# Optimization experiments

Measured on AMD Instinct MI355X. Metric: run time of the kernel, lower is better.

Reference implementation:

```python
import jax, jax.numpy as jnp
import numpy as np

# ---- static module config (HashEncoder defaults) ----
INPUT_DIM = 3
NUM_LEVELS = 16
LEVEL_DIM = 2
PER_LEVEL_SCALE = 2.0
BASE_RES = 16
LOG2_HASHMAP = 19
MAX_PARAMS = 2 ** LOG2_HASHMAP
S = np.log2(PER_LEVEL_SCALE)  # log2 of per-level scale, as in the CUDA kernel
B_POINTS = 1048576

# per-level table offsets, exactly as in HashEncoder.__init__
_offs = [0]
_off = 0
for _i in range(NUM_LEVELS):
    _res = int(np.ceil(BASE_RES * PER_LEVEL_SCALE ** _i))
    _p = min(MAX_PARAMS, (_res + 1) ** INPUT_DIM)
    _p = int(_p / 8) * 8
    _off += _p
    _offs.append(_off)
OFFSETS = np.array(_offs, dtype=np.int64)
N_ENTRIES = _off  # 7132272

# spatial hash primes from torch-ngp fast_hash (first 3 dims)
PRIMES = np.array([1, 2654435761, 805459861], dtype=np.uint32)


def _encode_level(inputs, emb_level, level, hashmap_size):
    """One resolution level: hash 8 corners, gather, trilinear-interp. inputs: [B,3] in [0,1]."""
    scale = np.float32(np.exp2(level * S) * BASE_RES - 1.0)
    resolution = int(np.ceil(scale)) + 1
    pos = inputs * scale + 0.5
    pos_grid = jnp.floor(pos)
    frac = pos - pos_grid                    # [B,3] trilinear fractions
    pg = pos_grid.astype(jnp.uint32)         # [B,3] base corner
    # kernel hashes whenever the dense grid would exceed the (rounded) table size
    use_hash = (resolution + 1) ** INPUT_DIM > hashmap_size
    hs = np.uint32(hashmap_size)
    out = jnp.zeros((inputs.shape[0], LEVEL_DIM), dtype=inputs.dtype)
    for c in range(2 ** INPUT_DIM):          # 8 corners
        bits = np.array([(c >> d) & 1 for d in range(INPUT_DIM)], dtype=np.uint32)
        w = jnp.prod(jnp.where(bits.astype(bool), frac, 1.0 - frac), axis=-1)  # [B]
        corner = pg + bits                   # [B,3] uint32
        if use_hash:
            h = corner * PRIMES              # uint32 wrap-around multiply
            idx = h[:, 0] ^ h[:, 1] ^ h[:, 2]
        else:
            stride = np.uint32(resolution + 1)
            idx = corner[:, 0] + corner[:, 1] * stride + corner[:, 2] * (stride * stride)
        idx = (idx % hs).astype(jnp.int32)
        out = out + w[:, None] * emb_level[idx]  # irregular gather [B,C]
    return out


def setup_inputs() -> dict:
    key = jax.random.key(0)
    k1, k2 = jax.random.split(key)
    xyz = jax.random.uniform(k1, (B_POINTS, INPUT_DIM), dtype=jnp.float32)
    # reset_parameters: uniform(-1e-4, 1e-4)
    embeddings = jax.random.uniform(k2, (N_ENTRIES, LEVEL_DIM), dtype=jnp.float32,
                                    minval=-1e-4, maxval=1e-4)
    return {"xyz": xyz, "embeddings": embeddings, "normalize": 0}


def reference(xyz, embeddings, normalize):
    # normalize == 0 -> use raw coords (kernel expects [0,1]^3), matching normalize=False path
    inputs = xyz.reshape(-1, INPUT_DIM)
    outs = []
    for l in range(NUM_LEVELS):
        o0, o1 = int(OFFSETS[l]), int(OFFSETS[l + 1])
        outs.append(_encode_level(inputs, embeddings[o0:o1], l, o1 - o0))
    # equivalent to outputs.permute(1,0,2).reshape(B, L*C)
    return jnp.concatenate(outs, axis=-1)
```

## Files before the change

kernel.cpp:

```cpp
#include <hip/hip_runtime.h>
#include <hip/hip_fp16.h>

#define NLEVELS 16
#define BLOCK 256
#define PPT1 4
#define PPT 2

struct HashParams {
    unsigned offs[NLEVELS + 1];
    unsigned hsize[NLEVELS];
    unsigned hash_bits;
    unsigned pow2_bits;
};

__global__ void __launch_bounds__(BLOCK)
hashenc_conv(const float4* __restrict__ emb2, uint2* __restrict__ tab16, int n2)
{
    const int i = blockIdx.x * BLOCK + threadIdx.x;
    if (i < n2) {
        const float4 v = emb2[i];
        const __half2 a = __floats2half2_rn(v.x, v.y);
        const __half2 b = __floats2half2_rn(v.z, v.w);
        tab16[i] = make_uint2(*(const unsigned*)&a, *(const unsigned*)&b);
    }
}

__global__ void __launch_bounds__(BLOCK)
hashenc_pass1_h(const float* __restrict__ xyz,
                const unsigned* __restrict__ tab16,
                unsigned* __restrict__ ws,
                HashParams p, int np, int bpl_shift)
{
    const int l = blockIdx.x >> bpl_shift;
    const int chunk = blockIdx.x & ((1 << bpl_shift) - 1);
    const int tid = threadIdx.x;

    __shared__ float sxyz[BLOCK * PPT1 * 3];
    {
        const float4* __restrict__ src =
            (const float4*)(xyz + (size_t)chunk * (BLOCK * PPT1) * 3);
        float4* __restrict__ dst = (float4*)sxyz;
#pragma unroll
        for (int i = tid; i < (BLOCK * PPT1 * 3) / 4; i += BLOCK)
            dst[i] = src[i];
    }
    __syncthreads();

    const unsigned hs = p.hsize[l];
    const unsigned* __restrict__ tab = tab16 + p.offs[l];
    const float scale = (float)((16u << l) - 1u);
    const bool is_pow2 = (p.pow2_bits >> l) & 1u;
    unsigned* __restrict__ wl = ws + (size_t)l * np;

    unsigned raw[PPT1][8];
    unsigned selba[PPT1];
    float fxa[PPT1], fya[PPT1], fza[PPT1];

#pragma unroll
    for (int s = 0; s < PPT1; ++s) {
        const int lp = s * BLOCK + tid;
        const float x = sxyz[lp * 3 + 0];
        const float y = sxyz[lp * 3 + 1];
        const float z = sxyz[lp * 3 + 2];
        const float px = x * scale + 0.5f;
        const float py = y * scale + 0.5f;
        const float pz = z * scale + 0.5f;
        const float gx = floorf(px), gy = floorf(py), gz = floorf(pz);
        fxa[s] = px - gx; fya[s] = py - gy; fza[s] = pz - gz;
        const unsigned ix = (unsigned)gx, iy = (unsigned)gy, iz = (unsigned)gz;

        const unsigned hy0 = iy * 2654435761u;
        const unsigned hz0 = iz * 805459861u;
        const unsigned hy1 = hy0 + 2654435761u;
        const unsigned hz1 = hz0 + 805459861u;
        const unsigned hyz[4] = { hy0 ^ hz0, hy1 ^ hz0, hy0 ^ hz1, hy1 ^ hz1 };

        unsigned selb = 0u;
        if (is_pow2) {
            const unsigned m = hs - 1u;
            if (!(ix & 1u)) {
#pragma unroll
                for (int q = 0; q < 4; ++q) {
                    const unsigned v0 = (ix ^ hyz[q]) & m;
                    const uint2 pr = *reinterpret_cast<const uint2*>(tab + (v0 & ~1u));
                    raw[s][2 * q]     = pr.x;
                    raw[s][2 * q + 1] = pr.y;
                    selb |= (v0 & 1u) << q;
                }
            } else {
#pragma unroll
                for (int q = 0; q < 4; ++q) {
                    raw[s][2 * q]     = tab[(ix ^ hyz[q]) & m];
                    raw[s][2 * q + 1] = tab[((ix + 1u) ^ hyz[q]) & m];
                }
            }
        } else {
#pragma unroll
            for (int q = 0; q < 4; ++q) {
                raw[s][2 * q]     = tab[(ix ^ hyz[q]) % hs];
                raw[s][2 * q + 1] = tab[((ix + 1u) ^ hyz[q]) % hs];
            }
        }
        selba[s] = selb;
    }

#pragma unroll
    for (int s = 0; s < PPT1; ++s) {
        const float fx = fxa[s], fy = fya[s], fz = fza[s];
        const float wxv[2] = {1.0f - fx, fx};
        const float wyv[2] = {1.0f - fy, fy};
        const float wzv[2] = {1.0f - fz, fz};
        const unsigned selb = selba[s];
        float o0 = 0.0f, o1 = 0.0f;
#pragma unroll
        for (int q = 0; q < 4; ++q) {
            const unsigned r0 = raw[s][2 * q], r1 = raw[s][2 * q + 1];
            const bool sw = (selb >> q) & 1u;
            const unsigned ua = sw ? r1 : r0;
            const unsigned ub = sw ? r0 : r1;
            const float2 ea = __half22float2(*reinterpret_cast<const __half2*>(&ua));
            const float2 eb = __half22float2(*reinterpret_cast<const __half2*>(&ub));
            const float wq = wyv[q & 1] * wzv[q >> 1];
            const float w0 = wxv[0] * wq, w1 = wxv[1] * wq;
            o0 = fmaf(w0, ea.x, o0); o1 = fmaf(w0, ea.y, o1);
            o0 = fmaf(w1, eb.x, o0); o1 = fmaf(w1, eb.y, o1);
        }
        const int pidx = chunk * (BLOCK * PPT1) + s * BLOCK + tid;
        const __half2 ph = __floats2half2_rn(o0, o1);
        wl[pidx] = *(const unsigned*)&ph;
    }
}

__global__ void __launch_bounds__(BLOCK)
hashenc_pass2_h(const unsigned* __restrict__ ws, float* __restrict__ out, int np)
{
    __shared__ float lds[BLOCK * 33];
    const int tid = threadIdx.x;
    const int p0 = blockIdx.x * BLOCK;

#pragma unroll
    for (int l = 0; l < NLEVELS; ++l) {
        const unsigned u = ws[(size_t)l * np + p0 + tid];
        const float2 v = __half22float2(*reinterpret_cast<const __half2*>(&u));
        lds[tid * 33 + 2 * l + 0] = v.x;
        lds[tid * 33 + 2 * l + 1] = v.y;
    }
    __syncthreads();
    float* __restrict__ ochunk = out + (size_t)blockIdx.x * (BLOCK * 32);
#pragma unroll
    for (int k = 0; k < 32; ++k) {
        const int flat = k * BLOCK + tid;
        const float v = lds[(flat >> 5) * 33 + (flat & 31)];
        __builtin_nontemporal_store(v, ochunk + flat);
    }
}

__global__ void __launch_bounds__(BLOCK)
hashenc_pass1_f32(const float* __restrict__ xyz,
                  const float* __restrict__ emb,
                  float2* __restrict__ ws,
                  HashParams p, int np, int bpl_shift)
{
    const int l = blockIdx.x >> bpl_shift;
    const int chunk = blockIdx.x & ((1 << bpl_shift) - 1);
    const int tid = threadIdx.x;

    __shared__ float sxyz[BLOCK * PPT * 3];
    {
        const float4* __restrict__ src =
            (const float4*)(xyz + (size_t)chunk * (BLOCK * PPT) * 3);
        float4* __restrict__ dst = (float4*)sxyz;
#pragma unroll
        for (int i = tid; i < (BLOCK * PPT * 3) / 4; i += BLOCK)
            dst[i] = src[i];
    }
    __syncthreads();

    const unsigned hs = p.hsize[l];
    const float2* __restrict__ tab = (const float2*)emb + p.offs[l];
    const float scale = (float)((16u << l) - 1u);
    const bool do_hash = (p.hash_bits >> l) & 1u;
    const bool is_pow2 = (p.pow2_bits >> l) & 1u;
    float2* __restrict__ wl = ws + (size_t)l * np;

#pragma unroll
    for (int s = 0; s < PPT; ++s) {
        const int lp = s * BLOCK + tid;
        const int pidx = chunk * (BLOCK * PPT) + lp;
        const float x = sxyz[lp * 3 + 0];
        const float y = sxyz[lp * 3 + 1];
        const float z = sxyz[lp * 3 + 2];
        const float px = x * scale + 0.5f;
        const float py = y * scale + 0.5f;
        const float pz = z * scale + 0.5f;
        const float gx = floorf(px), gy = floorf(py), gz = floorf(pz);
        const float fx = px - gx, fy = py - gy, fz = pz - gz;
        const unsigned ix = (unsigned)gx, iy = (unsigned)gy, iz = (unsigned)gz;
        const float wxv[2] = {1.0f - fx, fx};
        const float wyv[2] = {1.0f - fy, fy};
        const float wzv[2] = {1.0f - fz, fz};
        float o0 = 0.0f, o1 = 0.0f;
        unsigned idx[8];
        if (do_hash) {
            const unsigned hy0 = iy * 2654435761u;
            const unsigned hz0 = iz * 805459861u;
            const unsigned hy1 = hy0 + 2654435761u;
            const unsigned hz1 = hz0 + 805459861u;
            if (is_pow2) {
                const unsigned m = hs - 1u;
#pragma unroll
                for (int c = 0; c < 8; ++c)
                    idx[c] = ((ix + (c & 1)) ^ ((c & 2) ? hy1 : hy0) ^ ((c & 4) ? hz1 : hz0)) & m;
            } else {
#pragma unroll
                for (int c = 0; c < 8; ++c)
                    idx[c] = ((ix + (c & 1)) ^ ((c & 2) ? hy1 : hy0) ^ ((c & 4) ? hz1 : hz0)) % hs;
            }
        } else {
            const unsigned stride = (16u << l) + 1u;
#pragma unroll
            for (int c = 0; c < 8; ++c) {
                const unsigned lin = (ix + (c & 1))
                                   + (iy + ((c >> 1) & 1)) * stride
                                   + (iz + ((c >> 2) & 1)) * stride * stride;
                idx[c] = lin % hs;
            }
        }
        float2 e[8];
#pragma unroll
        for (int c = 0; c < 8; ++c) e[c] = tab[idx[c]];
#pragma unroll
        for (int c = 0; c < 8; ++c) {
            const float w = wxv[c & 1] * wyv[(c >> 1) & 1] * wzv[(c >> 2) & 1];
            o0 = fmaf(w, e[c].x, o0);
            o1 = fmaf(w, e[c].y, o1);
        }
        wl[pidx] = make_float2(o0, o1);
    }
}

__global__ void __launch_bounds__(BLOCK)
hashenc_pass2(const float2* __restrict__ ws, float* __restrict__ out, int np)
{
    __shared__ float lds[BLOCK * 33];
    const int tid = threadIdx.x;
    const int p0 = blockIdx.x * BLOCK;

#pragma unroll
    for (int l = 0; l < NLEVELS; ++l) {
        const float2 v = ws[(size_t)l * np + p0 + tid];
        lds[tid * 33 + 2 * l + 0] = v.x;
        lds[tid * 33 + 2 * l + 1] = v.y;
    }
    __syncthreads();
    float* __restrict__ ochunk = out + (size_t)blockIdx.x * (BLOCK * 32);
#pragma unroll
    for (int k = 0; k < 32; ++k) {
        const int flat = k * BLOCK + tid;
        const float v = lds[(flat >> 5) * 33 + (flat & 31)];
        __builtin_nontemporal_store(v, ochunk + flat);
    }
}

__global__ void __launch_bounds__(BLOCK)
hashenc_fwd(const float* __restrict__ xyz,
            const float* __restrict__ emb,
            float* __restrict__ out,
            HashParams p)
{
    const int tid = threadIdx.x;
    const long b = (long)blockIdx.x * BLOCK + tid;
    __shared__ float lds[BLOCK * 33];

    const float x = xyz[b * 3 + 0];
    const float y = xyz[b * 3 + 1];
    const float z = xyz[b * 3 + 2];

#pragma unroll
    for (int l = 0; l < NLEVELS; ++l) {
        const float scale = (float)((16u << l) - 1u);
        const float px = x * scale + 0.5f;
        const float py = y * scale + 0.5f;
        const float pz = z * scale + 0.5f;
        const float gx = floorf(px), gy = floorf(py), gz = floorf(pz);
        const float fx = px - gx, fy = py - gy, fz = pz - gz;
        const unsigned ix = (unsigned)gx, iy = (unsigned)gy, iz = (unsigned)gz;
        const unsigned hs = p.hsize[l];
        const float2* __restrict__ tab = (const float2*)emb + p.offs[l];

        unsigned idx[8];
        if ((p.hash_bits >> l) & 1u) {
            const unsigned hy0 = iy * 2654435761u;
            const unsigned hz0 = iz * 805459861u;
            const unsigned hy1 = hy0 + 2654435761u;
            const unsigned hz1 = hz0 + 805459861u;
            if ((p.pow2_bits >> l) & 1u) {
                const unsigned m = hs - 1u;
#pragma unroll
                for (int c = 0; c < 8; ++c)
                    idx[c] = ((ix + (c & 1)) ^ ((c & 2) ? hy1 : hy0) ^ ((c & 4) ? hz1 : hz0)) & m;
            } else {
#pragma unroll
                for (int c = 0; c < 8; ++c)
                    idx[c] = ((ix + (c & 1)) ^ ((c & 2) ? hy1 : hy0) ^ ((c & 4) ? hz1 : hz0)) % hs;
            }
        } else {
            const unsigned stride = (16u << l) + 1u;
#pragma unroll
            for (int c = 0; c < 8; ++c) {
                const unsigned lin = (ix + (c & 1))
                                   + (iy + ((c >> 1) & 1)) * stride
                                   + (iz + ((c >> 2) & 1)) * stride * stride;
                idx[c] = lin % hs;
            }
        }

        float2 e[8];
#pragma unroll
        for (int c = 0; c < 8; ++c) e[c] = tab[idx[c]];

        const float wx[2] = {1.0f - fx, fx};
        const float wy[2] = {1.0f - fy, fy};
        const float wz[2] = {1.0f - fz, fz};
        float o0 = 0.0f, o1 = 0.0f;
#pragma unroll
        for (int c = 0; c < 8; ++c) {
            const float w = wx[c & 1] * wy[(c >> 1) & 1] * wz[(c >> 2) & 1];
            o0 = fmaf(w, e[c].x, o0);
            o1 = fmaf(w, e[c].y, o1);
        }
        lds[tid * 33 + l * 2 + 0] = o0;
        lds[tid * 33 + l * 2 + 1] = o1;
    }

    __syncthreads();
    float* __restrict__ ochunk = out + (long)blockIdx.x * (BLOCK * 32);
#pragma unroll
    for (int k = 0; k < 32; ++k) {
        const int flat = k * BLOCK + tid;
        const float v = lds[(flat >> 5) * 33 + (flat & 31)];
        __builtin_nontemporal_store(v, ochunk + flat);
    }
}

extern "C" void kernel_launch(void* const* d_in, const int* in_sizes, int n_in,
                              void* d_out, int out_size, void* d_ws, size_t ws_size,
                              hipStream_t stream) {
    const float* xyz = (const float*)d_in[0];
    const float* emb = (const float*)d_in[1];
    float* out = (float*)d_out;
    const int B = in_sizes[0] / 3;

    HashParams p;
    p.offs[0] = 0;
    unsigned hash_bits = 0, pow2_bits = 0;
    long off = 0;
    for (int i = 0; i < NLEVELS; ++i) {
        const long res = 16L << i;
        const long dense = (res + 1) * (res + 1) * (res + 1);
        long t = dense < (1L << 19) ? dense : (1L << 19);
        t = (t / 8) * 8;
        p.hsize[i] = (unsigned)t;
        off += t;
        p.offs[i + 1] = (unsigned)off;
        if (dense > t) hash_bits |= (1u << i);
        if ((t & (t - 1)) == 0) pow2_bits |= (1u << i);
    }
    p.hash_bits = hash_bits;
    p.pow2_bits = pow2_bits;

    const long nent = off;
    const size_t need_ws16 = (size_t)B * NLEVELS * 4;
    const size_t need_h = need_ws16 + (size_t)nent * 4;
    const size_t need_f32 = (size_t)B * NLEVELS * sizeof(float2);
    const bool shape1_ok = (B % (BLOCK * PPT1)) == 0 && (B % BLOCK) == 0;
    const bool shape2_ok = (B % (BLOCK * PPT)) == 0 && (B % BLOCK) == 0;
    const bool all_hashed = (hash_bits == ((1u << NLEVELS) - 1u));

    if (shape1_ok && all_hashed && ws_size >= need_h) {
        unsigned* tab16 = (unsigned*)((char*)d_ws + need_ws16);
        const int n2 = (int)(nent / 2);
        hashenc_conv<<<dim3((n2 + BLOCK - 1) / BLOCK), dim3(BLOCK), 0, stream>>>(
            (const float4*)emb, (uint2*)tab16, n2);
        int bpl_shift = 0;
        while ((1 << bpl_shift) * (BLOCK * PPT1) < B) ++bpl_shift;
        const int bpl = 1 << bpl_shift;
        hashenc_pass1_h<<<dim3(NLEVELS * bpl), dim3(BLOCK), 0, stream>>>(
            xyz, tab16, (unsigned*)d_ws, p, B, bpl_shift);
        hashenc_pass2_h<<<dim3(B / BLOCK), dim3(BLOCK), 0, stream>>>(
            (const unsigned*)d_ws, out, B);
    } else if (shape2_ok && ws_size >= need_f32) {
        int bpl_shift = 0;
        while ((1 << bpl_shift) * (BLOCK * PPT) < B) ++bpl_shift;
        const int bpl = 1 << bpl_shift;
        hashenc_pass1_f32<<<dim3(NLEVELS * bpl), dim3(BLOCK), 0, stream>>>(
            xyz, emb, (float2*)d_ws, p, B, bpl_shift);
        hashenc_pass2<<<dim3(B / BLOCK), dim3(BLOCK), 0, stream>>>(
            (const float2*)d_ws, out, B);
    } else {
        hashenc_fwd<<<dim3(B / BLOCK), dim3(BLOCK), 0, stream>>>(xyz, emb, out, p);
    }
}
```

Before: 485.9 us.

## Encode two coarsest levels with LDS-staged hash table chunks in separate kernel

Adds a kernel that handles levels 0 and 1 by staging each level's fp16 table in 12288-entry chunks in shared memory. Every point scans all chunks and accumulates only the corners whose index falls inside the current chunk. The main per-level kernel now starts at level 2 and launches fewer blocks. The aim is to replace scattered global gathers on the small coarse tables with LDS reads, at the cost of recomputing hashes and reloading xyz from global memory once per chunk, plus one extra kernel launch.

Result: slower. 503.2 us (+3.6%).

```diff
diff --git a/kernel.cpp b/kernel.cpp
--- a/kernel.cpp
+++ b/kernel.cpp
@@ -5,6 +5,9 @@
 #define BLOCK 256
 #define PPT1 4
 #define PPT 2
+#define CCHUNK 12288
+#define PPT_C 8
+#define NCOARSE 2
 
 struct HashParams {
     unsigned offs[NLEVELS + 1];
@@ -26,12 +29,90 @@
 }
 
 __global__ void __launch_bounds__(BLOCK)
+hashenc_coarse(const float* __restrict__ xyz,
+               const unsigned* __restrict__ tab16,
+               unsigned* __restrict__ ws,
+               HashParams p, int np, int cblk_shift)
+{
+    __shared__ unsigned stab[CCHUNK];
+    const int l = blockIdx.x >> cblk_shift;
+    const int blk = blockIdx.x & ((1 << cblk_shift) - 1);
+    const int tid = threadIdx.x;
+
+    const unsigned hs = p.hsize[l];
+    const unsigned* __restrict__ tab = tab16 + p.offs[l];
+    const float scale = (float)((16u << l) - 1u);
+    unsigned* __restrict__ wl = ws + (size_t)l * np;
+    const int nchunks = (int)((hs + CCHUNK - 1) / CCHUNK);
+    const int base = blk * (BLOCK * PPT_C);
+
+    float acc0[PPT_C], acc1[PPT_C];
+#pragma unroll
+    for (int s = 0; s < PPT_C; ++s) { acc0[s] = 0.0f; acc1[s] = 0.0f; }
+
+    for (int c = 0; c < nchunks; ++c) {
+        const unsigned c0 = (unsigned)c * CCHUNK;
+        const unsigned cend = (c0 + CCHUNK < hs) ? c0 + CCHUNK : hs;
+        __syncthreads();
+        for (int i = tid; i < (int)(cend - c0); i += BLOCK)
+            stab[i] = tab[c0 + i];
+        __syncthreads();
+
+#pragma unroll
+        for (int s = 0; s < PPT_C; ++s) {
+            const int pidx = base + s * BLOCK + tid;
+            const float x = xyz[pidx * 3 + 0];
+            const float y = xyz[pidx * 3 + 1];
+            const float z = xyz[pidx * 3 + 2];
+            const float px = x * scale + 0.5f;
+            const float py = y * scale + 0.5f;
+            const float pz = z * scale + 0.5f;
+            const float gx = floorf(px), gy = floorf(py), gz = floorf(pz);
+            const float fx = px - gx, fy = py - gy, fz = pz - gz;
+            const unsigned ix = (unsigned)gx, iy = (unsigned)gy, iz = (unsigned)gz;
+            const unsigned hy0 = iy * 2654435761u;
+            const unsigned hz0 = iz * 805459861u;
+            const unsigned hy1 = hy0 + 2654435761u;
+            const unsigned hz1 = hz0 + 805459861u;
+            const unsigned hyz[4] = { hy0 ^ hz0, hy1 ^ hz0, hy0 ^ hz1, hy1 ^ hz1 };
+            const float wxv[2] = {1.0f - fx, fx};
+            const float wyv[2] = {1.0f - fy, fy};
+            const float wzv[2] = {1.0f - fz, fz};
+            float o0 = acc0[s], o1 = acc1[s];
+#pragma unroll
+            for (int q = 0; q < 4; ++q) {
+                const float wq = wyv[q & 1] * wzv[q >> 1];
+#pragma unroll
+                for (int cx = 0; cx < 2; ++cx) {
+                    const unsigned idx = ((ix + (unsigned)cx) ^ hyz[q]) % hs;
+                    if (idx >= c0 && idx < cend) {
+                        const unsigned u = stab[idx - c0];
+                        const float2 e = __half22float2(*reinterpret_cast<const __half2*>(&u));
+                        const float w = wxv[cx] * wq;
+                        o0 = fmaf(w, e.x, o0);
+                        o1 = fmaf(w, e.y, o1);
+                    }
+                }
+            }
+            acc0[s] = o0; acc1[s] = o1;
+        }
+    }
+
+#pragma unroll
+    for (int s = 0; s < PPT_C; ++s) {
+        const int pidx = base + s * BLOCK + tid;
+        const __half2 ph = __floats2half2_rn(acc0[s], acc1[s]);
+        wl[pidx] = *(const unsigned*)&ph;
+    }
+}
+
+__global__ void __launch_bounds__(BLOCK)
 hashenc_pass1_h(const float* __restrict__ xyz,
                 const unsigned* __restrict__ tab16,
                 unsigned* __restrict__ ws,
                 HashParams p, int np, int bpl_shift)
 {
-    const int l = blockIdx.x >> bpl_shift;
+    const int l = NCOARSE + (blockIdx.x >> bpl_shift);
     const int chunk = blockIdx.x & ((1 << bpl_shift) - 1);
     const int tid = threadIdx.x;
 
@@ -373,20 +454,28 @@
     const size_t need_ws16 = (size_t)B * NLEVELS * 4;
     const size_t need_h = need_ws16 + (size_t)nent * 4;
     const size_t need_f32 = (size_t)B * NLEVELS * sizeof(float2);
-    const bool shape1_ok = (B % (BLOCK * PPT1)) == 0 && (B % BLOCK) == 0;
+    const bool shape1_ok = (B % (BLOCK * PPT1)) == 0 && (B % (BLOCK * PPT_C)) == 0
+                        && (B % BLOCK) == 0;
     const bool shape2_ok = (B % (BLOCK * PPT)) == 0 && (B % BLOCK) == 0;
     const bool all_hashed = (hash_bits == ((1u << NLEVELS) - 1u));
-
-    if (shape1_ok && all_hashed && ws_size >= need_h) {
+    const bool coarse_ok = p.hsize[0] <= 4u * CCHUNK && p.hsize[1] <= 4u * CCHUNK;
+
+    if (shape1_ok && all_hashed && coarse_ok && ws_size >= need_h) {
         unsigned* tab16 = (unsigned*)((char*)d_ws + need_ws16);
         const int n2 = (int)(nent / 2);
         hashenc_conv<<<dim3((n2 + BLOCK - 1) / BLOCK), dim3(BLOCK), 0, stream>>>(
             (const float4*)emb, (uint2*)tab16, n2);
+
+        int cblk_shift = 0;
+        while ((1 << cblk_shift) * (BLOCK * PPT_C) < B) ++cblk_shift;
+        hashenc_coarse<<<dim3(NCOARSE << cblk_shift), dim3(BLOCK), 0, stream>>>(
+            xyz, tab16, (unsigned*)d_ws, p, B, cblk_shift);
+
         int bpl_shift = 0;
         while ((1 << bpl_shift) * (BLOCK * PPT1) < B) ++bpl_shift;
-        const int bpl = 1 << bpl_shift;
-        hashenc_pass1_h<<<dim3(NLEVELS * bpl), dim3(BLOCK), 0, stream>>>(
+        hashenc_pass1_h<<<dim3((NLEVELS - NCOARSE) << bpl_shift), dim3(BLOCK), 0, stream>>>(
             xyz, tab16, (unsigned*)d_ws, p, B, bpl_shift);
+
         hashenc_pass2_h<<<dim3(B / BLOCK), dim3(BLOCK), 0, stream>>>(
             (const unsigned*)d_ws, out, B);
     } else if (shape2_ok && ws_size >= need_f32) {
```
